# Performance work log

Measured on AMD Instinct MI355X. Metric: run time of the kernel, lower is better.

The kernel has to match this reference:

```python
import jax, jax.numpy as jnp
import numpy as np

ALPHAS = (0.1, 0.3, 0.6)
WEIGHTS = (0.5, 0.3, 0.2)
HUBER_MARGIN = 1.0
B, S = 2048, 8192


def setup_inputs() -> dict:
    key = jax.random.key(0)
    k1, k2 = jax.random.split(key)
    pred = jax.random.normal(k1, (B, S), dtype=jnp.float32)
    target = jax.random.normal(k2, (B, S), dtype=jnp.float32)
    return {"pred": pred, "target": target}


def _ema(x, alpha):
    # x: [B, S]; ema[0] = x[0]; ema[i] = alpha*x[i] + (1-alpha)*ema[i-1]
    x0 = x[:, 0]
    def step(carry, xi):
        nc = alpha * xi + (1.0 - alpha) * carry
        return nc, nc
    _, ys = jax.lax.scan(step, x0, x[:, 1:].T)  # ys: [S-1, B]
    return jnp.concatenate([x0[:, None], ys.T], axis=1)  # [B, S]


def _huber_loss(pred_delta, target_delta):
    dir_agreement = pred_delta * target_delta
    step_err = jnp.abs(pred_delta - target_delta)
    quad = jnp.square(jnp.maximum(HUBER_MARGIN - dir_agreement, 0.0)) / (2.0 * HUBER_MARGIN)
    return jnp.where(dir_agreement < 0, step_err, quad).mean(axis=1)  # [B]


def reference(pred, target):
    loss = jnp.zeros((pred.shape[0],), dtype=pred.dtype)
    for alpha, weight in zip(ALPHAS, WEIGHTS):
        pe = _ema(pred, alpha)
        te = _ema(target, alpha)
        pd = pe[:, 1:] - pe[:, :-1]
        td = te[:, 1:] - te[:, :-1]
        loss = loss + weight * _huber_loss(pd, td)
    return loss.mean()  # reduction='mean'
```

## Files before the change

kernel.cpp:

```cpp
#include <hip/hip_runtime.h>

#define B_ROWS 2048
#define S_LEN 8192
#define SEG_OUT 1024
#define WARM 256
#define EXT (SEG_OUT + WARM)
#define PER_LANE 20
#define NSEG (S_LEN / SEG_OUT)
#define WPB 4
#define NBLOCKS (B_ROWS * NSEG / WPB)

constexpr double cpowi(double b, int e) { double r = 1.0; for (int i = 0; i < e; ++i) r *= b; return r; }
constexpr float trim(double x) { return (x < 1e-12 && x > -1e-12) ? 0.0f : (float)x; }

#define A0f 0.1f
#define A1f 0.3f
#define A2f 0.6f

constexpr float D0_1 = trim(cpowi(0.9, 20)),  D0_2 = trim(cpowi(0.9, 40)),  D0_4 = trim(cpowi(0.9, 80));
constexpr float D0_8 = trim(cpowi(0.9, 160)), D0_16 = trim(cpowi(0.9, 320)), D0_32 = trim(cpowi(0.9, 640));
constexpr float D1_1 = trim(cpowi(0.7, 20)),  D1_2 = trim(cpowi(0.7, 40)),  D1_4 = trim(cpowi(0.7, 80));
constexpr float D1_8 = trim(cpowi(0.7, 160)), D1_16 = trim(cpowi(0.7, 320)), D1_32 = trim(cpowi(0.7, 640));
constexpr float D2_1 = trim(cpowi(0.4, 20)),  D2_2 = trim(cpowi(0.4, 40)),  D2_4 = trim(cpowi(0.4, 80));
constexpr float D2_8 = trim(cpowi(0.4, 160)), D2_16 = trim(cpowi(0.4, 320)), D2_32 = trim(cpowi(0.4, 640));

__device__ __forceinline__ float ema_scan(float v, int lane,
                                          float d1, float d2, float d4,
                                          float d8, float d16, float d32) {
    float u;
    if (d1 != 0.0f) { u = __shfl_up(v, 1);  v += (lane >= 1  ? d1  : 0.0f) * u; }
    if (d2 != 0.0f) { u = __shfl_up(v, 2);  v += (lane >= 2  ? d2  : 0.0f) * u; }
    if (d4 != 0.0f) { u = __shfl_up(v, 4);  v += (lane >= 4  ? d4  : 0.0f) * u; }
    if (d8 != 0.0f) { u = __shfl_up(v, 8);  v += (lane >= 8  ? d8  : 0.0f) * u; }
    if (d16 != 0.0f) { u = __shfl_up(v, 16); v += (lane >= 16 ? d16 : 0.0f) * u; }
    if (d32 != 0.0f) { u = __shfl_up(v, 32); v += (lane >= 32 ? d32 : 0.0f) * u; }
    return v;
}

__device__ __forceinline__ float huber(float pd, float td) {
    float dir = pd * td;
    float se  = fabsf(pd - td);
    float mm  = fmaxf(1.0f - dir, 0.0f);
    float q   = 0.5f * mm * mm;
    return dir < 0.0f ? se : q;
}

#define PASS1(px, tx)                                         \
    Lp0 += A0f * ((px) - Lp0); Lp1 += A1f * ((px) - Lp1);     \
    Lp2 += A2f * ((px) - Lp2);                                \
    Lt0 += A0f * ((tx) - Lt0); Lt1 += A1f * ((tx) - Lt1);     \
    Lt2 += A2f * ((tx) - Lt2);

#define PASS2(px, tx, J) {                                    \
    float pd0 = A0f * ((px) - yp0); yp0 += pd0;               \
    float td0 = A0f * ((tx) - yt0); yt0 += td0;               \
    float pd1 = A1f * ((px) - yp1); yp1 += pd1;               \
    float td1 = A1f * ((tx) - yt1); yt1 += td1;               \
    float pd2 = A2f * ((px) - yp2); yp2 += pd2;               \
    float td2 = A2f * ((tx) - yt2); yt2 += td2;               \
    const int e_ = ebase + (J);                               \
    const float m_ = (e_ >= lo && e_ < hi) ? 1.0f : 0.0f;     \
    acc0 += m_ * huber(pd0, td0);                             \
    acc1 += m_ * huber(pd1, td1);                             \
    acc2 += m_ * huber(pd2, td2); }

__global__ void __launch_bounds__(256, 4) msl_main(const float* __restrict__ pred,
                                                   const float* __restrict__ targ,
                                                   float* __restrict__ out) {
    const int lane = threadIdx.x & 63;
    const int wave = threadIdx.x >> 6;
    const int g    = blockIdx.x * WPB + wave;
    const int row  = g >> 3;
    const int seg  = g & 7;
    const bool s0  = (seg == 0);
    const bool lz  = (lane == 0);

    const int ext_base = s0 ? 0 : seg * SEG_OUT - WARM;
    const int lo = s0 ? 1 : WARM;
    const int hi = s0 ? SEG_OUT : EXT;

    const float* __restrict__ prow = pred + (size_t)row * S_LEN + ext_base + lane * PER_LANE;
    const float* __restrict__ trow = targ + (size_t)row * S_LEN + ext_base + lane * PER_LANE;

    const float4* p4 = reinterpret_cast<const float4*>(prow);
    const float4* t4 = reinterpret_cast<const float4*>(trow);
    float4 p0 = p4[0], p1 = p4[1], p2 = p4[2], p3 = p4[3], p5 = p4[4];
    float4 t0 = t4[0], t1 = t4[1], t2 = t4[2], t3 = t4[3], t5 = t4[4];

    const float ip = (lz && s0) ? p0.x : 0.0f;
    const float it = (lz && s0) ? t0.x : 0.0f;
    float Lp0 = ip, Lp1 = ip, Lp2 = ip;
    float Lt0 = it, Lt1 = it, Lt2 = it;

    PASS1(p0.x, t0.x) PASS1(p0.y, t0.y) PASS1(p0.z, t0.z) PASS1(p0.w, t0.w)
    PASS1(p1.x, t1.x) PASS1(p1.y, t1.y) PASS1(p1.z, t1.z) PASS1(p1.w, t1.w)
    PASS1(p2.x, t2.x) PASS1(p2.y, t2.y) PASS1(p2.z, t2.z) PASS1(p2.w, t2.w)
    PASS1(p3.x, t3.x) PASS1(p3.y, t3.y) PASS1(p3.z, t3.z) PASS1(p3.w, t3.w)
    PASS1(p5.x, t5.x) PASS1(p5.y, t5.y) PASS1(p5.z, t5.z) PASS1(p5.w, t5.w)

    float vp0 = ema_scan(Lp0, lane, D0_1, D0_2, D0_4, D0_8, D0_16, D0_32);
    float vp1 = ema_scan(Lp1, lane, D1_1, D1_2, D1_4, D1_8, D1_16, D1_32);
    float vp2 = ema_scan(Lp2, lane, D2_1, D2_2, D2_4, D2_8, D2_16, D2_32);
    float vt0 = ema_scan(Lt0, lane, D0_1, D0_2, D0_4, D0_8, D0_16, D0_32);
    float vt1 = ema_scan(Lt1, lane, D1_1, D1_2, D1_4, D1_8, D1_16, D1_32);
    float vt2 = ema_scan(Lt2, lane, D2_1, D2_2, D2_4, D2_8, D2_16, D2_32);

    float cp0 = __shfl_up(vp0, 1), cp1 = __shfl_up(vp1, 1), cp2 = __shfl_up(vp2, 1);
    float ct0 = __shfl_up(vt0, 1), ct1 = __shfl_up(vt1, 1), ct2 = __shfl_up(vt2, 1);

    float yp0 = lz ? ip : cp0;
    float yp1 = lz ? ip : cp1;
    float yp2 = lz ? ip : cp2;
    float yt0 = lz ? it : ct0;
    float yt1 = lz ? it : ct1;
    float yt2 = lz ? it : ct2;

    float acc0 = 0.f, acc1 = 0.f, acc2 = 0.f;
    const int ebase = lane * PER_LANE;

    PASS2(p0.x, t0.x, 0)  PASS2(p0.y, t0.y, 1)  PASS2(p0.z, t0.z, 2)  PASS2(p0.w, t0.w, 3)
    PASS2(p1.x, t1.x, 4)  PASS2(p1.y, t1.y, 5)  PASS2(p1.z, t1.z, 6)  PASS2(p1.w, t1.w, 7)
    PASS2(p2.x, t2.x, 8)  PASS2(p2.y, t2.y, 9)  PASS2(p2.z, t2.z, 10) PASS2(p2.w, t2.w, 11)
    PASS2(p3.x, t3.x, 12) PASS2(p3.y, t3.y, 13) PASS2(p3.z, t3.z, 14) PASS2(p3.w, t3.w, 15)
    PASS2(p5.x, t5.x, 16) PASS2(p5.y, t5.y, 17) PASS2(p5.z, t5.z, 18) PASS2(p5.w, t5.w, 19)

    float wacc = 0.5f * acc0 + 0.3f * acc1 + 0.2f * acc2;
#pragma unroll
    for (int o = 32; o > 0; o >>= 1) wacc += __shfl_down(wacc, o);

    __shared__ float sred[WPB];
    if (lz) sred[wave] = wacc;
    __syncthreads();
    if (threadIdx.x == 0) {
        const float scale = (float)(1.0 / ((double)(S_LEN - 1) * (double)B_ROWS));
        atomicAdd(out, (sred[0] + sred[1] + sred[2] + sred[3]) * scale);
    }
}

extern "C" void kernel_launch(void* const* d_in, const int* in_sizes, int n_in,
                              void* d_out, int out_size, void* d_ws, size_t ws_size,
                              hipStream_t stream) {
    const float* pred = (const float*)d_in[0];
    const float* targ = (const float*)d_in[1];
    float* out = (float*)d_out;

    hipMemsetAsync(out, 0, sizeof(float), stream);
    msl_main<<<NBLOCKS, 256, 0, stream>>>(pred, targ, out);
}
```

Before: 173.1 us.

## Process each segment in three 512-element tiles with carried EMA state

Each wave now walks its extended segment as three tiles of 8 elements per lane, carrying the EMA state between tiles through a lane-63 broadcast instead of holding 20 elements per lane in one scan. The warm-up is raised to 512 and the scan decay constants are recomputed for the 8-element chunk, with a looser trim threshold. Smaller per-lane state is meant to lower register pressure (launch bounds raised to 5 blocks) and to let the next tile's loads be issued during compute. The cost is three sets of wave-wide scans per segment and more redundant warm-up reads. Segment 0 skips the last tile's Huber pass and other segments skip the first.

```diff
diff --git a/kernel.cpp b/kernel.cpp
--- a/kernel.cpp
+++ b/kernel.cpp
@@ -3,26 +3,28 @@
 #define B_ROWS 2048
 #define S_LEN 8192
 #define SEG_OUT 1024
-#define WARM 256
+#define WARM 512
 #define EXT (SEG_OUT + WARM)
-#define PER_LANE 20
+#define CHUNK 8
+#define TILE (64 * CHUNK)
+#define NTILE (EXT / TILE)
 #define NSEG (S_LEN / SEG_OUT)
 #define WPB 4
 #define NBLOCKS (B_ROWS * NSEG / WPB)
 
 constexpr double cpowi(double b, int e) { double r = 1.0; for (int i = 0; i < e; ++i) r *= b; return r; }
-constexpr float trim(double x) { return (x < 1e-12 && x > -1e-12) ? 0.0f : (float)x; }
+constexpr float trim(double x) { return (x < 1e-8 && x > -1e-8) ? 0.0f : (float)x; }
 
 #define A0f 0.1f
 #define A1f 0.3f
 #define A2f 0.6f
 
-constexpr float D0_1 = trim(cpowi(0.9, 20)),  D0_2 = trim(cpowi(0.9, 40)),  D0_4 = trim(cpowi(0.9, 80));
-constexpr float D0_8 = trim(cpowi(0.9, 160)), D0_16 = trim(cpowi(0.9, 320)), D0_32 = trim(cpowi(0.9, 640));
-constexpr float D1_1 = trim(cpowi(0.7, 20)),  D1_2 = trim(cpowi(0.7, 40)),  D1_4 = trim(cpowi(0.7, 80));
-constexpr float D1_8 = trim(cpowi(0.7, 160)), D1_16 = trim(cpowi(0.7, 320)), D1_32 = trim(cpowi(0.7, 640));
-constexpr float D2_1 = trim(cpowi(0.4, 20)),  D2_2 = trim(cpowi(0.4, 40)),  D2_4 = trim(cpowi(0.4, 80));
-constexpr float D2_8 = trim(cpowi(0.4, 160)), D2_16 = trim(cpowi(0.4, 320)), D2_32 = trim(cpowi(0.4, 640));
+constexpr float E0_1 = trim(cpowi(0.9, 8)),   E0_2 = trim(cpowi(0.9, 16)),  E0_4 = trim(cpowi(0.9, 32));
+constexpr float E0_8 = trim(cpowi(0.9, 64)),  E0_16 = trim(cpowi(0.9, 128)), E0_32 = trim(cpowi(0.9, 256));
+constexpr float E1_1 = trim(cpowi(0.7, 8)),   E1_2 = trim(cpowi(0.7, 16)),  E1_4 = trim(cpowi(0.7, 32));
+constexpr float E1_8 = trim(cpowi(0.7, 64)),  E1_16 = trim(cpowi(0.7, 128)), E1_32 = trim(cpowi(0.7, 256));
+constexpr float E2_1 = trim(cpowi(0.4, 8)),   E2_2 = trim(cpowi(0.4, 16)),  E2_4 = trim(cpowi(0.4, 32));
+constexpr float E2_8 = trim(cpowi(0.4, 64)),  E2_16 = trim(cpowi(0.4, 128)), E2_32 = trim(cpowi(0.4, 256));
 
 __device__ __forceinline__ float ema_scan(float v, int lane,
                                           float d1, float d2, float d4,
@@ -58,13 +60,47 @@
     float td1 = A1f * ((tx) - yt1); yt1 += td1;               \
     float pd2 = A2f * ((px) - yp2); yp2 += pd2;               \
     float td2 = A2f * ((tx) - yt2); yt2 += td2;               \
-    const int e_ = ebase + (J);                               \
-    const float m_ = (e_ >= lo && e_ < hi) ? 1.0f : 0.0f;     \
+    const float m_ = ((ebase + (J)) >= lo) ? 1.0f : 0.0f;     \
     acc0 += m_ * huber(pd0, td0);                             \
     acc1 += m_ * huber(pd1, td1);                             \
     acc2 += m_ * huber(pd2, td2); }
 
-__global__ void __launch_bounds__(256, 4) msl_main(const float* __restrict__ pred,
+__device__ __forceinline__ void do_tile(
+    float4 A0, float4 A1, float4 B0, float4 B1,
+    int lane, bool lz, int ebase, int lo, bool run2,
+    float& sp0, float& sp1, float& sp2,
+    float& st0, float& st1, float& st2,
+    float& acc0, float& acc1, float& acc2)
+{
+    float Lp0 = lz ? sp0 : 0.f, Lp1 = lz ? sp1 : 0.f, Lp2 = lz ? sp2 : 0.f;
+    float Lt0 = lz ? st0 : 0.f, Lt1 = lz ? st1 : 0.f, Lt2 = lz ? st2 : 0.f;
+    PASS1(A0.x, B0.x) PASS1(A0.y, B0.y) PASS1(A0.z, B0.z) PASS1(A0.w, B0.w)
+    PASS1(A1.x, B1.x) PASS1(A1.y, B1.y) PASS1(A1.z, B1.z) PASS1(A1.w, B1.w)
+
+    float vp0 = ema_scan(Lp0, lane, E0_1, E0_2, E0_4, E0_8, E0_16, E0_32);
+    float vp1 = ema_scan(Lp1, lane, E1_1, E1_2, E1_4, E1_8, E1_16, E1_32);
+    float vp2 = ema_scan(Lp2, lane, E2_1, E2_2, E2_4, E2_8, E2_16, E2_32);
+    float vt0 = ema_scan(Lt0, lane, E0_1, E0_2, E0_4, E0_8, E0_16, E0_32);
+    float vt1 = ema_scan(Lt1, lane, E1_1, E1_2, E1_4, E1_8, E1_16, E1_32);
+    float vt2 = ema_scan(Lt2, lane, E2_1, E2_2, E2_4, E2_8, E2_16, E2_32);
+
+    float yp0 = lz ? sp0 : __shfl_up(vp0, 1);
+    float yp1 = lz ? sp1 : __shfl_up(vp1, 1);
+    float yp2 = lz ? sp2 : __shfl_up(vp2, 1);
+    float yt0 = lz ? st0 : __shfl_up(vt0, 1);
+    float yt1 = lz ? st1 : __shfl_up(vt1, 1);
+    float yt2 = lz ? st2 : __shfl_up(vt2, 1);
+
+    sp0 = __shfl(vp0, 63); sp1 = __shfl(vp1, 63); sp2 = __shfl(vp2, 63);
+    st0 = __shfl(vt0, 63); st1 = __shfl(vt1, 63); st2 = __shfl(vt2, 63);
+
+    if (run2) {
+        PASS2(A0.x, B0.x, 0) PASS2(A0.y, B0.y, 1) PASS2(A0.z, B0.z, 2) PASS2(A0.w, B0.w, 3)
+        PASS2(A1.x, B1.x, 4) PASS2(A1.y, B1.y, 5) PASS2(A1.z, B1.z, 6) PASS2(A1.w, B1.w, 7)
+    }
+}
+
+__global__ void __launch_bounds__(256, 5) msl_main(const float* __restrict__ pred,
                                                    const float* __restrict__ targ,
                                                    float* __restrict__ out) {
     const int lane = threadIdx.x & 63;
@@ -77,52 +113,35 @@
 
     const int ext_base = s0 ? 0 : seg * SEG_OUT - WARM;
     const int lo = s0 ? 1 : WARM;
-    const int hi = s0 ? SEG_OUT : EXT;
 
-    const float* __restrict__ prow = pred + (size_t)row * S_LEN + ext_base + lane * PER_LANE;
-    const float* __restrict__ trow = targ + (size_t)row * S_LEN + ext_base + lane * PER_LANE;
-
+    const float* __restrict__ prow = pred + (size_t)row * S_LEN + ext_base;
+    const float* __restrict__ trow = targ + (size_t)row * S_LEN + ext_base;
     const float4* p4 = reinterpret_cast<const float4*>(prow);
     const float4* t4 = reinterpret_cast<const float4*>(trow);
-    float4 p0 = p4[0], p1 = p4[1], p2 = p4[2], p3 = p4[3], p5 = p4[4];
-    float4 t0 = t4[0], t1 = t4[1], t2 = t4[2], t3 = t4[3], t5 = t4[4];
+    const int fo = lane * 2;
 
-    const float ip = (lz && s0) ? p0.x : 0.0f;
-    const float it = (lz && s0) ? t0.x : 0.0f;
-    float Lp0 = ip, Lp1 = ip, Lp2 = ip;
-    float Lt0 = it, Lt1 = it, Lt2 = it;
+    float sp0 = 0.f, sp1 = 0.f, sp2 = 0.f, st0 = 0.f, st1 = 0.f, st2 = 0.f;
+    float acc0 = 0.f, acc1 = 0.f, acc2 = 0.f;
 
-    PASS1(p0.x, t0.x) PASS1(p0.y, t0.y) PASS1(p0.z, t0.z) PASS1(p0.w, t0.w)
-    PASS1(p1.x, t1.x) PASS1(p1.y, t1.y) PASS1(p1.z, t1.z) PASS1(p1.w, t1.w)
-    PASS1(p2.x, t2.x) PASS1(p2.y, t2.y) PASS1(p2.z, t2.z) PASS1(p2.w, t2.w)
-    PASS1(p3.x, t3.x) PASS1(p3.y, t3.y) PASS1(p3.z, t3.z) PASS1(p3.w, t3.w)
-    PASS1(p5.x, t5.x) PASS1(p5.y, t5.y) PASS1(p5.z, t5.z) PASS1(p5.w, t5.w)
+    float4 A0 = p4[fo], A1 = p4[fo + 1];
+    float4 B0 = t4[fo], B1 = t4[fo + 1];
+    float4 nA0 = p4[128 + fo], nA1 = p4[128 + fo + 1];
+    float4 nB0 = t4[128 + fo], nB1 = t4[128 + fo + 1];
 
-    float vp0 = ema_scan(Lp0, lane, D0_1, D0_2, D0_4, D0_8, D0_16, D0_32);
-    float vp1 = ema_scan(Lp1, lane, D1_1, D1_2, D1_4, D1_8, D1_16, D1_32);
-    float vp2 = ema_scan(Lp2, lane, D2_1, D2_2, D2_4, D2_8, D2_16, D2_32);
-    float vt0 = ema_scan(Lt0, lane, D0_1, D0_2, D0_4, D0_8, D0_16, D0_32);
-    float vt1 = ema_scan(Lt1, lane, D1_1, D1_2, D1_4, D1_8, D1_16, D1_32);
-    float vt2 = ema_scan(Lt2, lane, D2_1, D2_2, D2_4, D2_8, D2_16, D2_32);
+    if (s0 && lz) { sp0 = sp1 = sp2 = A0.x; st0 = st1 = st2 = B0.x; }
 
-    float cp0 = __shfl_up(vp0, 1), cp1 = __shfl_up(vp1, 1), cp2 = __shfl_up(vp2, 1);
-    float ct0 = __shfl_up(vt0, 1), ct1 = __shfl_up(vt1, 1), ct2 = __shfl_up(vt2, 1);
+    do_tile(A0, A1, B0, B1, lane, lz, lane * CHUNK, lo, s0,
+            sp0, sp1, sp2, st0, st1, st2, acc0, acc1, acc2);
 
-    float yp0 = lz ? ip : cp0;
-    float yp1 = lz ? ip : cp1;
-    float yp2 = lz ? ip : cp2;
-    float yt0 = lz ? it : ct0;
-    float yt1 = lz ? it : ct1;
-    float yt2 = lz ? it : ct2;
+    A0 = nA0; A1 = nA1; B0 = nB0; B1 = nB1;
+    nA0 = p4[256 + fo]; nA1 = p4[256 + fo + 1];
+    nB0 = t4[256 + fo]; nB1 = t4[256 + fo + 1];
 
-    float acc0 = 0.f, acc1 = 0.f, acc2 = 0.f;
-    const int ebase = lane * PER_LANE;
+    do_tile(A0, A1, B0, B1, lane, lz, TILE + lane * CHUNK, lo, true,
+            sp0, sp1, sp2, st0, st1, st2, acc0, acc1, acc2);
 
-    PASS2(p0.x, t0.x, 0)  PASS2(p0.y, t0.y, 1)  PASS2(p0.z, t0.z, 2)  PASS2(p0.w, t0.w, 3)
-    PASS2(p1.x, t1.x, 4)  PASS2(p1.y, t1.y, 5)  PASS2(p1.z, t1.z, 6)  PASS2(p1.w, t1.w, 7)
-    PASS2(p2.x, t2.x, 8)  PASS2(p2.y, t2.y, 9)  PASS2(p2.z, t2.z, 10) PASS2(p2.w, t2.w, 11)
-    PASS2(p3.x, t3.x, 12) PASS2(p3.y, t3.y, 13) PASS2(p3.z, t3.z, 14) PASS2(p3.w, t3.w, 15)
-    PASS2(p5.x, t5.x, 16) PASS2(p5.y, t5.y, 17) PASS2(p5.z, t5.z, 18) PASS2(p5.w, t5.w, 19)
+    do_tile(nA0, nA1, nB0, nB1, lane, lz, 2 * TILE + lane * CHUNK, lo, !s0,
+            sp0, sp1, sp2, st0, st1, st2, acc0, acc1, acc2);
 
     float wacc = 0.5f * acc0 + 0.3f * acc1 + 0.2f * acc2;
 #pragma unroll
```

Measured after the change: 173.3 us. Within noise of the previous version (+0.1%).

## Process full rows per wave with carried EMA state instead of overlapping warm-up segments

Applied to the files above, without the earlier changes.

Each wave now handles an entire row in four sequential 2048-element tiles, carrying the EMA state across tiles through a lane-63 broadcast. This replaces the earlier scheme of eight segments per row, each reading a 256-element warm-up overlap, so the 25% redundant loads and compute go away. Loads are double-buffered in registers, with the next tile fetched while the current one is computed. The costs are fewer, longer-running waves, a serial dependency between tiles, and much higher register pressure, with launch bounds lowered to 2 blocks per CU, which reduces the parallelism available to hide memory latency.

```diff
diff --git a/kernel.cpp b/kernel.cpp
--- a/kernel.cpp
+++ b/kernel.cpp
@@ -2,13 +2,11 @@
 
 #define B_ROWS 2048
 #define S_LEN 8192
-#define SEG_OUT 1024
-#define WARM 256
-#define EXT (SEG_OUT + WARM)
-#define PER_LANE 20
-#define NSEG (S_LEN / SEG_OUT)
+#define PER_LANE 32
+#define TILE_ELEMS (64 * PER_LANE)
+#define NTILES (S_LEN / TILE_ELEMS)
 #define WPB 4
-#define NBLOCKS (B_ROWS * NSEG / WPB)
+#define NBLOCKS (B_ROWS / WPB)
 
 constexpr double cpowi(double b, int e) { double r = 1.0; for (int i = 0; i < e; ++i) r *= b; return r; }
 constexpr float trim(double x) { return (x < 1e-12 && x > -1e-12) ? 0.0f : (float)x; }
@@ -17,12 +15,12 @@
 #define A1f 0.3f
 #define A2f 0.6f
 
-constexpr float D0_1 = trim(cpowi(0.9, 20)),  D0_2 = trim(cpowi(0.9, 40)),  D0_4 = trim(cpowi(0.9, 80));
-constexpr float D0_8 = trim(cpowi(0.9, 160)), D0_16 = trim(cpowi(0.9, 320)), D0_32 = trim(cpowi(0.9, 640));
-constexpr float D1_1 = trim(cpowi(0.7, 20)),  D1_2 = trim(cpowi(0.7, 40)),  D1_4 = trim(cpowi(0.7, 80));
-constexpr float D1_8 = trim(cpowi(0.7, 160)), D1_16 = trim(cpowi(0.7, 320)), D1_32 = trim(cpowi(0.7, 640));
-constexpr float D2_1 = trim(cpowi(0.4, 20)),  D2_2 = trim(cpowi(0.4, 40)),  D2_4 = trim(cpowi(0.4, 80));
-constexpr float D2_8 = trim(cpowi(0.4, 160)), D2_16 = trim(cpowi(0.4, 320)), D2_32 = trim(cpowi(0.4, 640));
+constexpr float D0_1 = trim(cpowi(0.9, 32)),  D0_2 = trim(cpowi(0.9, 64)),  D0_4 = trim(cpowi(0.9, 128));
+constexpr float D0_8 = trim(cpowi(0.9, 256)), D0_16 = trim(cpowi(0.9, 512)), D0_32 = trim(cpowi(0.9, 1024));
+constexpr float D1_1 = trim(cpowi(0.7, 32)),  D1_2 = trim(cpowi(0.7, 64)),  D1_4 = trim(cpowi(0.7, 128));
+constexpr float D1_8 = trim(cpowi(0.7, 256)), D1_16 = trim(cpowi(0.7, 512)), D1_32 = trim(cpowi(0.7, 1024));
+constexpr float D2_1 = trim(cpowi(0.4, 32)),  D2_2 = trim(cpowi(0.4, 64)),  D2_4 = trim(cpowi(0.4, 128));
+constexpr float D2_8 = trim(cpowi(0.4, 256)), D2_16 = trim(cpowi(0.4, 512)), D2_32 = trim(cpowi(0.4, 1024));
 
 __device__ __forceinline__ float ema_scan(float v, int lane,
                                           float d1, float d2, float d4,
@@ -45,84 +43,93 @@
     return dir < 0.0f ? se : q;
 }
 
-#define PASS1(px, tx)                                         \
-    Lp0 += A0f * ((px) - Lp0); Lp1 += A1f * ((px) - Lp1);     \
-    Lp2 += A2f * ((px) - Lp2);                                \
-    Lt0 += A0f * ((tx) - Lt0); Lt1 += A1f * ((tx) - Lt1);     \
-    Lt2 += A2f * ((tx) - Lt2);
+#define LOADT(T, XP, XT) {                                                     \
+    const float4* p4_ = reinterpret_cast<const float4*>(prow + (T) * TILE_ELEMS); \
+    const float4* t4_ = reinterpret_cast<const float4*>(trow + (T) * TILE_ELEMS); \
+    _Pragma("unroll")                                                          \
+    for (int j = 0; j < PER_LANE / 4; ++j) {                                   \
+        float4 a_ = p4_[fo + j]; float4 b_ = t4_[fo + j];                      \
+        XP[4*j+0] = a_.x; XP[4*j+1] = a_.y; XP[4*j+2] = a_.z; XP[4*j+3] = a_.w; \
+        XT[4*j+0] = b_.x; XT[4*j+1] = b_.y; XT[4*j+2] = b_.z; XT[4*j+3] = b_.w; } }
 
-#define PASS2(px, tx, J) {                                    \
-    float pd0 = A0f * ((px) - yp0); yp0 += pd0;               \
-    float td0 = A0f * ((tx) - yt0); yt0 += td0;               \
-    float pd1 = A1f * ((px) - yp1); yp1 += pd1;               \
-    float td1 = A1f * ((tx) - yt1); yt1 += td1;               \
-    float pd2 = A2f * ((px) - yp2); yp2 += pd2;               \
-    float td2 = A2f * ((tx) - yt2); yt2 += td2;               \
-    const int e_ = ebase + (J);                               \
-    const float m_ = (e_ >= lo && e_ < hi) ? 1.0f : 0.0f;     \
-    acc0 += m_ * huber(pd0, td0);                             \
-    acc1 += m_ * huber(pd1, td1);                             \
-    acc2 += m_ * huber(pd2, td2); }
+#define COMPUTE(XP, XT, FIRST) {                                               \
+    float Lp0, Lp1, Lp2, Lt0, Lt1, Lt2;                                        \
+    if (FIRST) {                                                               \
+        const float icp_ = lz ? XP[0] : 0.0f;                                  \
+        const float ict_ = lz ? XT[0] : 0.0f;                                  \
+        Lp0 = Lp1 = Lp2 = icp_; Lt0 = Lt1 = Lt2 = ict_;                        \
+    } else {                                                                   \
+        Lp0 = lz ? sp0 : 0.f; Lp1 = lz ? sp1 : 0.f; Lp2 = lz ? sp2 : 0.f;      \
+        Lt0 = lz ? st0 : 0.f; Lt1 = lz ? st1 : 0.f; Lt2 = lz ? st2 : 0.f;      \
+    }                                                                          \
+    _Pragma("unroll")                                                          \
+    for (int j = 0; j < PER_LANE; ++j) {                                       \
+        Lp0 += A0f * (XP[j] - Lp0); Lp1 += A1f * (XP[j] - Lp1);                \
+        Lp2 += A2f * (XP[j] - Lp2);                                            \
+        Lt0 += A0f * (XT[j] - Lt0); Lt1 += A1f * (XT[j] - Lt1);                \
+        Lt2 += A2f * (XT[j] - Lt2);                                            \
+    }                                                                          \
+    float vp0 = ema_scan(Lp0, lane, D0_1, D0_2, D0_4, D0_8, D0_16, D0_32);     \
+    float vp1 = ema_scan(Lp1, lane, D1_1, D1_2, D1_4, D1_8, D1_16, D1_32);     \
+    float vp2 = ema_scan(Lp2, lane, D2_1, D2_2, D2_4, D2_8, D2_16, D2_32);     \
+    float vt0 = ema_scan(Lt0, lane, D0_1, D0_2, D0_4, D0_8, D0_16, D0_32);     \
+    float vt1 = ema_scan(Lt1, lane, D1_1, D1_2, D1_4, D1_8, D1_16, D1_32);     \
+    float vt2 = ema_scan(Lt2, lane, D2_1, D2_2, D2_4, D2_8, D2_16, D2_32);     \
+    float yp0, yp1, yp2, yt0, yt1, yt2;                                        \
+    {                                                                          \
+        float cp0 = __shfl_up(vp0, 1), cp1 = __shfl_up(vp1, 1), cp2 = __shfl_up(vp2, 1); \
+        float ct0 = __shfl_up(vt0, 1), ct1 = __shfl_up(vt1, 1), ct2 = __shfl_up(vt2, 1); \
+        if (FIRST) {                                                           \
+            yp0 = lz ? XP[0] : cp0; yp1 = lz ? XP[0] : cp1; yp2 = lz ? XP[0] : cp2; \
+            yt0 = lz ? XT[0] : ct0; yt1 = lz ? XT[0] : ct1; yt2 = lz ? XT[0] : ct2; \
+        } else {                                                               \
+            yp0 = lz ? sp0 : cp0; yp1 = lz ? sp1 : cp1; yp2 = lz ? sp2 : cp2;  \
+            yt0 = lz ? st0 : ct0; yt1 = lz ? st1 : ct1; yt2 = lz ? st2 : ct2;  \
+        }                                                                      \
+    }                                                                          \
+    sp0 = __shfl(vp0, 63); sp1 = __shfl(vp1, 63); sp2 = __shfl(vp2, 63);       \
+    st0 = __shfl(vt0, 63); st1 = __shfl(vt1, 63); st2 = __shfl(vt2, 63);       \
+    const float skip_ = (FIRST && lz) ? 0.0f : 1.0f;                           \
+    _Pragma("unroll")                                                          \
+    for (int j = 0; j < PER_LANE; ++j) {                                       \
+        float pd0 = A0f * (XP[j] - yp0); yp0 += pd0;                           \
+        float td0 = A0f * (XT[j] - yt0); yt0 += td0;                           \
+        float pd1 = A1f * (XP[j] - yp1); yp1 += pd1;                           \
+        float td1 = A1f * (XT[j] - yt1); yt1 += td1;                           \
+        float pd2 = A2f * (XP[j] - yp2); yp2 += pd2;                           \
+        float td2 = A2f * (XT[j] - yt2); yt2 += td2;                           \
+        float h0 = huber(pd0, td0);                                            \
+        float h1 = huber(pd1, td1);                                            \
+        float h2 = huber(pd2, td2);                                            \
+        if (j == 0) { h0 *= skip_; h1 *= skip_; h2 *= skip_; }                 \
+        acc0 += h0; acc1 += h1; acc2 += h2;                                    \
+    } }
 
-__global__ void __launch_bounds__(256, 4) msl_main(const float* __restrict__ pred,
+__global__ void __launch_bounds__(256, 2) msl_main(const float* __restrict__ pred,
                                                    const float* __restrict__ targ,
                                                    float* __restrict__ out) {
     const int lane = threadIdx.x & 63;
     const int wave = threadIdx.x >> 6;
-    const int g    = blockIdx.x * WPB + wave;
-    const int row  = g >> 3;
-    const int seg  = g & 7;
-    const bool s0  = (seg == 0);
+    const int row  = blockIdx.x * WPB + wave;
     const bool lz  = (lane == 0);
+    const int fo   = lane * (PER_LANE / 4);
 
-    const int ext_base = s0 ? 0 : seg * SEG_OUT - WARM;
-    const int lo = s0 ? 1 : WARM;
-    const int hi = s0 ? SEG_OUT : EXT;
+    const float* __restrict__ prow = pred + (size_t)row * S_LEN;
+    const float* __restrict__ trow = targ + (size_t)row * S_LEN;
 
-    const float* __restrict__ prow = pred + (size_t)row * S_LEN + ext_base + lane * PER_LANE;
-    const float* __restrict__ trow = targ + (size_t)row * S_LEN + ext_base + lane * PER_LANE;
+    float sp0 = 0.f, sp1 = 0.f, sp2 = 0.f, st0 = 0.f, st1 = 0.f, st2 = 0.f;
+    float acc0 = 0.f, acc1 = 0.f, acc2 = 0.f;
 
-    const float4* p4 = reinterpret_cast<const float4*>(prow);
-    const float4* t4 = reinterpret_cast<const float4*>(trow);
-    float4 p0 = p4[0], p1 = p4[1], p2 = p4[2], p3 = p4[3], p5 = p4[4];
-    float4 t0 = t4[0], t1 = t4[1], t2 = t4[2], t3 = t4[3], t5 = t4[4];
+    float xpa[PER_LANE], xta[PER_LANE], xpb[PER_LANE], xtb[PER_LANE];
 
-    const float ip = (lz && s0) ? p0.x : 0.0f;
-    const float it = (lz && s0) ? t0.x : 0.0f;
-    float Lp0 = ip, Lp1 = ip, Lp2 = ip;
-    float Lt0 = it, Lt1 = it, Lt2 = it;
-
-    PASS1(p0.x, t0.x) PASS1(p0.y, t0.y) PASS1(p0.z, t0.z) PASS1(p0.w, t0.w)
-    PASS1(p1.x, t1.x) PASS1(p1.y, t1.y) PASS1(p1.z, t1.z) PASS1(p1.w, t1.w)
-    PASS1(p2.x, t2.x) PASS1(p2.y, t2.y) PASS1(p2.z, t2.z) PASS1(p2.w, t2.w)
-    PASS1(p3.x, t3.x) PASS1(p3.y, t3.y) PASS1(p3.z, t3.z) PASS1(p3.w, t3.w)
-    PASS1(p5.x, t5.x) PASS1(p5.y, t5.y) PASS1(p5.z, t5.z) PASS1(p5.w, t5.w)
-
-    float vp0 = ema_scan(Lp0, lane, D0_1, D0_2, D0_4, D0_8, D0_16, D0_32);
-    float vp1 = ema_scan(Lp1, lane, D1_1, D1_2, D1_4, D1_8, D1_16, D1_32);
-    float vp2 = ema_scan(Lp2, lane, D2_1, D2_2, D2_4, D2_8, D2_16, D2_32);
-    float vt0 = ema_scan(Lt0, lane, D0_1, D0_2, D0_4, D0_8, D0_16, D0_32);
-    float vt1 = ema_scan(Lt1, lane, D1_1, D1_2, D1_4, D1_8, D1_16, D1_32);
-    float vt2 = ema_scan(Lt2, lane, D2_1, D2_2, D2_4, D2_8, D2_16, D2_32);
-
-    float cp0 = __shfl_up(vp0, 1), cp1 = __shfl_up(vp1, 1), cp2 = __shfl_up(vp2, 1);
-    float ct0 = __shfl_up(vt0, 1), ct1 = __shfl_up(vt1, 1), ct2 = __shfl_up(vt2, 1);
-
-    float yp0 = lz ? ip : cp0;
-    float yp1 = lz ? ip : cp1;
-    float yp2 = lz ? ip : cp2;
-    float yt0 = lz ? it : ct0;
-    float yt1 = lz ? it : ct1;
-    float yt2 = lz ? it : ct2;
-
-    float acc0 = 0.f, acc1 = 0.f, acc2 = 0.f;
-    const int ebase = lane * PER_LANE;
-
-    PASS2(p0.x, t0.x, 0)  PASS2(p0.y, t0.y, 1)  PASS2(p0.z, t0.z, 2)  PASS2(p0.w, t0.w, 3)
-    PASS2(p1.x, t1.x, 4)  PASS2(p1.y, t1.y, 5)  PASS2(p1.z, t1.z, 6)  PASS2(p1.w, t1.w, 7)
-    PASS2(p2.x, t2.x, 8)  PASS2(p2.y, t2.y, 9)  PASS2(p2.z, t2.z, 10) PASS2(p2.w, t2.w, 11)
-    PASS2(p3.x, t3.x, 12) PASS2(p3.y, t3.y, 13) PASS2(p3.z, t3.z, 14) PASS2(p3.w, t3.w, 15)
-    PASS2(p5.x, t5.x, 16) PASS2(p5.y, t5.y, 17) PASS2(p5.z, t5.z, 18) PASS2(p5.w, t5.w, 19)
+    LOADT(0, xpa, xta)
+    LOADT(1, xpb, xtb)
+    COMPUTE(xpa, xta, 1)
+    LOADT(2, xpa, xta)
+    COMPUTE(xpb, xtb, 0)
+    LOADT(3, xpb, xtb)
+    COMPUTE(xpa, xta, 0)
+    COMPUTE(xpb, xtb, 0)
 
     float wacc = 0.5f * acc0 + 0.3f * acc1 + 0.2f * acc2;
 #pragma unroll
```

After: 169.3 us. -2.2%, faster.
